# Kernel tuning notes

Hardware: AMD Instinct MI355X
Metric: run time of the kernel (lower is better)

Reference implementation:

```python
import jax, jax.numpy as jnp
import numpy as np

N = 100000    # nodes
R = 8         # relations
HFR = 128     # input feature dim
HTO = 128     # output feature dim
NNZ = 1600000 # edges (nonzeros of the (N*R, N) sparse matrix)


def setup_inputs() -> dict:
    key = jax.random.key(0)
    k1, k2, k3, k4, k5 = jax.random.split(key, 5)
    nodes = jax.random.normal(k1, (N, HFR), dtype=jnp.float32)
    rows = jax.random.randint(k2, (NNZ,), 0, N * R)   # row index into (N*R, N) sparse matrix
    cols = jax.random.randint(k3, (NNZ,), 0, N)       # column = source node
    indices = jnp.stack([rows, cols]).astype(jnp.int64)
    values = jax.random.uniform(k4, (NNZ,), dtype=jnp.float32)
    # xavier-uniform-ish init for (r, hfr, hto) relation weights
    weights = jax.random.normal(k5, (R, HFR, HTO), dtype=jnp.float32) * np.float32(1.0 / np.sqrt(HFR))
    return {"nodes": nodes, "indices": indices, "values": values, "weights": weights}


def reference(nodes, indices, values, weights):
    # nodes: [n, hfr]; indices: [2, nnz]; values: [nnz]; weights: [r, hfr, hto]
    n = nodes.shape[0]
    r = weights.shape[0]
    rows, cols = indices[0], indices[1]
    # spmm: (n*r, n) sparse @ (n, hfr) dense -> (n*r, hfr)
    msgs = values[:, None] * nodes[cols]                      # [nnz, hfr] gather + scale
    agg = jax.ops.segment_sum(msgs, rows, num_segments=n * r)  # [n*r, hfr] scatter-add
    agg = agg.reshape(r, n, -1)                                # [r, n, hfr]
    # per-relation GEMM 'rij,rnj->nri' followed by sum over r, fused into one einsum
    out = jnp.einsum('rij,rnj->ni', weights, agg)              # [n, hto]
    return jax.nn.relu(out)
```

## Files before the change

kernel.cpp:

```cpp
#include <hip/hip_runtime.h>
#include <hip/hip_bf16.h>
#include <stdint.h>

#define HFR 128
#define HTO 128
#define LDN 136

typedef short short8 __attribute__((ext_vector_type(8)));
typedef float f32x4  __attribute__((ext_vector_type(4)));
typedef unsigned long long u64;

static __device__ __forceinline__ unsigned short f2bf(float x) {
    __hip_bfloat16 h = __float2bfloat16(x);
    return *reinterpret_cast<unsigned short*>(&h);
}
static __device__ __forceinline__ float bflo(unsigned int x) {
    return __uint_as_float(x << 16);
}
static __device__ __forceinline__ float bfhi(unsigned int x) {
    return __uint_as_float(x & 0xffff0000u);
}

__global__ __launch_bounds__(256) void zero_i32(int* __restrict__ p, int n) {
    int i = blockIdx.x * 256 + threadIdx.x;
    if (i < n) p[i] = 0;
}

__global__ __launch_bounds__(256)
void count_kernel(const int* __restrict__ rows, int* __restrict__ cnt,
                  int N, int nnz) {
    int e = blockIdx.x * 256 + threadIdx.x;
    if (e >= nnz) return;
    int row = rows[e];
    int r   = row / N;
    int dst = row - r * N;
    atomicAdd(&cnt[dst], 1);
}

__global__ __launch_bounds__(256)
void scan_reduce(const int* __restrict__ cnt, int* __restrict__ bsum, int N) {
    __shared__ int s[256];
    int t = threadIdx.x;
    int i = blockIdx.x * 256 + t;
    s[t] = (i < N) ? cnt[i] : 0;
    __syncthreads();
    for (int off = 128; off > 0; off >>= 1) {
        if (t < off) s[t] += s[t + off];
        __syncthreads();
    }
    if (t == 0) bsum[blockIdx.x] = s[0];
}

__global__ __launch_bounds__(1024)
void scan_block(int* __restrict__ bsum, int nb) {
    __shared__ int s[1024];
    int t = threadIdx.x;
    s[t] = (t < nb) ? bsum[t] : 0;
    __syncthreads();
    for (int off = 1; off < 1024; off <<= 1) {
        int o = (t >= off) ? s[t - off] : 0;
        __syncthreads();
        s[t] += o;
        __syncthreads();
    }
    if (t < nb) bsum[t] = (t == 0) ? 0 : s[t - 1];
}

__global__ __launch_bounds__(256)
void scan_final(int* __restrict__ cnt, const int* __restrict__ bsum, int N) {
    __shared__ int s[256];
    int t = threadIdx.x;
    int i = blockIdx.x * 256 + t;
    int v = (i < N) ? cnt[i] : 0;
    s[t] = v;
    __syncthreads();
    for (int off = 1; off < 256; off <<= 1) {
        int o = (t >= off) ? s[t - off] : 0;
        __syncthreads();
        s[t] += o;
        __syncthreads();
    }
    int ex = ((t == 0) ? 0 : s[t - 1]) + bsum[blockIdx.x];
    if (i < N) cnt[i] = ex;
}

__global__ __launch_bounds__(256, 2)
void fused_tp(const float* __restrict__ nodes,
              const float* __restrict__ weights,
              __hip_bfloat16* __restrict__ H,
              const int* __restrict__ rows, const int* __restrict__ cols,
              const float* __restrict__ vals,
              int* __restrict__ cursor, u64* __restrict__ sorted,
              int N, int R, int nnz, int Tblocks) {
    __shared__ unsigned short nd[128 * LDN];
    __shared__ unsigned short wt[128 * LDN];

    if ((int)blockIdx.x >= Tblocks) {
        int e = (blockIdx.x - Tblocks) * 256 + threadIdx.x;
        if (e >= nnz) return;
        int row = rows[e];
        int r   = row / N;
        int dst = row - r * N;
        int pos = atomicAdd(&cursor[dst], 1);
        unsigned int lo = (unsigned int)cols[e] | ((unsigned int)r << 17);
        u64 rec = ((u64)__float_as_uint(vals[e]) << 32) | (u64)lo;
        sorted[pos] = rec;
        return;
    }

    const int t    = threadIdx.x;
    const int n0   = blockIdx.x * 128;
    const int lane = t & 63;
    const int w    = t >> 6;
    const int m    = lane & 15;
    const int quad = lane >> 4;
    const int q8   = quad * 8;
    const int w32  = w * 32;

    const float4* src4 = reinterpret_cast<const float4*>(nodes);
#pragma unroll
    for (int it = 0; it < 8; ++it) {
        int id  = t + 256 * it;
        int row = id >> 4;
        int k8  = id & 15;
        float4 v0 = make_float4(0.f, 0.f, 0.f, 0.f);
        float4 v1 = v0;
        if (n0 + row < N) {
            v0 = src4[(size_t)(n0 + row) * 32 + k8 * 2];
            v1 = src4[(size_t)(n0 + row) * 32 + k8 * 2 + 1];
        }
        short8 sv;
        sv[0] = f2bf(v0.x); sv[1] = f2bf(v0.y); sv[2] = f2bf(v0.z); sv[3] = f2bf(v0.w);
        sv[4] = f2bf(v1.x); sv[5] = f2bf(v1.y); sv[6] = f2bf(v1.z); sv[7] = f2bf(v1.w);
        *reinterpret_cast<short8*>(&nd[row * LDN + k8 * 8]) = sv;
    }

    for (int r = 0; r < R; ++r) {
        __syncthreads();
        const float4* wsrc = reinterpret_cast<const float4*>(weights + (size_t)r * HFR * HTO);
#pragma unroll
        for (int it = 0; it < 8; ++it) {
            int id  = t + 256 * it;
            int row = id >> 4;
            int k8  = id & 15;
            float4 v0 = wsrc[row * 32 + k8 * 2];
            float4 v1 = wsrc[row * 32 + k8 * 2 + 1];
            short8 sv;
            sv[0] = f2bf(v0.x); sv[1] = f2bf(v0.y); sv[2] = f2bf(v0.z); sv[3] = f2bf(v0.w);
            sv[4] = f2bf(v1.x); sv[5] = f2bf(v1.y); sv[6] = f2bf(v1.z); sv[7] = f2bf(v1.w);
            *reinterpret_cast<short8*>(&wt[row * LDN + k8 * 8]) = sv;
        }
        __syncthreads();

        f32x4 acc[2][8];
#pragma unroll
        for (int t2 = 0; t2 < 2; ++t2)
#pragma unroll
            for (int j = 0; j < 8; ++j) acc[t2][j] = (f32x4)(0.f);

#pragma unroll
        for (int kk = 0; kk < HFR; kk += 32) {
            short8 a0 = *reinterpret_cast<const short8*>(&nd[(w32 +      m) * LDN + kk + q8]);
            short8 a1 = *reinterpret_cast<const short8*>(&nd[(w32 + 16 + m) * LDN + kk + q8]);
#pragma unroll
            for (int j = 0; j < 8; ++j) {
                short8 b = *reinterpret_cast<const short8*>(&wt[(j * 16 + m) * LDN + kk + q8]);
                acc[0][j] = __builtin_amdgcn_mfma_f32_16x16x32_bf16(a0, b, acc[0][j], 0, 0, 0);
                acc[1][j] = __builtin_amdgcn_mfma_f32_16x16x32_bf16(a1, b, acc[1][j], 0, 0, 0);
            }
        }

#pragma unroll
        for (int t2 = 0; t2 < 2; ++t2) {
            int rowbase = n0 + w32 + t2 * 16 + quad * 4;
#pragma unroll
            for (int reg = 0; reg < 4; ++reg) {
                int n = rowbase + reg;
                if (n < N) {
                    __hip_bfloat16* dst = H + ((size_t)r * N + n) * HTO + m;
#pragma unroll
                    for (int j = 0; j < 8; ++j)
                        dst[j * 16] = __float2bfloat16(acc[t2][j][reg]);
                }
            }
        }
    }
}

__global__ __launch_bounds__(256)
void gather_kernel(const u64* __restrict__ sorted,
                   const int* __restrict__ cursor,
                   const __hip_bfloat16* __restrict__ H,
                   float* __restrict__ out, int N) {
    const int wave = threadIdx.x >> 6;
    const int lane = threadIdx.x & 63;
    const int n = blockIdx.x * 4 + wave;
    if (n >= N) return;

    int e         = (n == 0) ? 0 : cursor[n - 1];
    const int end = cursor[n];

    float a0 = 0.f, a1 = 0.f, b0 = 0.f, b1 = 0.f;
    float c0 = 0.f, c1 = 0.f, d0 = 0.f, d1 = 0.f;

    const unsigned short* Hu = reinterpret_cast<const unsigned short*>(H);

#define HROW(q) reinterpret_cast<const unsigned int*>( \
        Hu + ((((size_t)((unsigned int)(q) >> 17) & 7) * (size_t)N + \
               ((unsigned int)(q) & 0x1FFFF)) << 7))
#define VAL(q)  __uint_as_float((unsigned int)((q) >> 32))

    for (; e + 8 <= end; e += 8) {
        const u64* p = sorted + __builtin_amdgcn_readfirstlane(e);
        u64 q0 = p[0], q1 = p[1], q2 = p[2], q3 = p[3];
        u64 q4 = p[4], q5 = p[5], q6 = p[6], q7 = p[7];
        unsigned int x0 = HROW(q0)[lane];
        unsigned int x1 = HROW(q1)[lane];
        unsigned int x2 = HROW(q2)[lane];
        unsigned int x3 = HROW(q3)[lane];
        unsigned int x4 = HROW(q4)[lane];
        unsigned int x5 = HROW(q5)[lane];
        unsigned int x6 = HROW(q6)[lane];
        unsigned int x7 = HROW(q7)[lane];
        a0 = fmaf(bflo(x0), VAL(q0), a0); a1 = fmaf(bfhi(x0), VAL(q0), a1);
        b0 = fmaf(bflo(x1), VAL(q1), b0); b1 = fmaf(bfhi(x1), VAL(q1), b1);
        c0 = fmaf(bflo(x2), VAL(q2), c0); c1 = fmaf(bfhi(x2), VAL(q2), c1);
        d0 = fmaf(bflo(x3), VAL(q3), d0); d1 = fmaf(bfhi(x3), VAL(q3), d1);
        a0 = fmaf(bflo(x4), VAL(q4), a0); a1 = fmaf(bfhi(x4), VAL(q4), a1);
        b0 = fmaf(bflo(x5), VAL(q5), b0); b1 = fmaf(bfhi(x5), VAL(q5), b1);
        c0 = fmaf(bflo(x6), VAL(q6), c0); c1 = fmaf(bfhi(x6), VAL(q6), c1);
        d0 = fmaf(bflo(x7), VAL(q7), d0); d1 = fmaf(bfhi(x7), VAL(q7), d1);
    }
    for (; e + 2 <= end; e += 2) {
        const u64* p = sorted + __builtin_amdgcn_readfirstlane(e);
        u64 q0 = p[0], q1 = p[1];
        unsigned int x0 = HROW(q0)[lane];
        unsigned int x1 = HROW(q1)[lane];
        a0 = fmaf(bflo(x0), VAL(q0), a0); a1 = fmaf(bfhi(x0), VAL(q0), a1);
        b0 = fmaf(bflo(x1), VAL(q1), b0); b1 = fmaf(bfhi(x1), VAL(q1), b1);
    }
    if (e < end) {
        u64 q0 = sorted[e];
        unsigned int x0 = HROW(q0)[lane];
        a0 = fmaf(bflo(x0), VAL(q0), a0); a1 = fmaf(bfhi(x0), VAL(q0), a1);
    }
#undef HROW
#undef VAL

    float2 o;
    o.x = fmaxf(a0 + b0 + c0 + d0, 0.f);
    o.y = fmaxf(a1 + b1 + c1 + d1, 0.f);
    *reinterpret_cast<float2*>(out + (size_t)n * HTO + lane * 2) = o;
}

extern "C" void kernel_launch(void* const* d_in, const int* in_sizes, int n_in,
                              void* d_out, int out_size, void* d_ws, size_t ws_size,
                              hipStream_t stream) {
    const float* nodes   = (const float*)d_in[0];
    const int*   indices = (const int*)d_in[1];
    const float* vals    = (const float*)d_in[2];
    const float* weights = (const float*)d_in[3];

    const int N   = in_sizes[0] / HFR;
    const int nnz = in_sizes[1] / 2;
    const int R   = in_sizes[3] / (HFR * HTO);

    const int* rows = indices;
    const int* cols = indices + nnz;

    char* ws = (char*)d_ws;
    __hip_bfloat16* H = (__hip_bfloat16*)ws;
    size_t off = (size_t)R * N * HTO * sizeof(__hip_bfloat16);
    u64* sorted = (u64*)(ws + off);
    off += (size_t)nnz * sizeof(u64);
    int* cnt = (int*)(ws + off);
    off += (size_t)N * sizeof(int);
    int* bsum = (int*)(ws + off);

    float* out = (float*)d_out;

    const int NB = (N + 255) / 256;
    const int Tblocks = (N + 127) / 128;
    const int Pblocks = (nnz + 255) / 256;

    zero_i32<<<NB, 256, 0, stream>>>(cnt, N);
    count_kernel<<<Pblocks, 256, 0, stream>>>(rows, cnt, N, nnz);
    scan_reduce<<<NB, 256, 0, stream>>>(cnt, bsum, N);
    scan_block<<<1, 1024, 0, stream>>>(bsum, NB);
    scan_final<<<NB, 256, 0, stream>>>(cnt, bsum, N);
    fused_tp<<<Tblocks + Pblocks, 256, 0, stream>>>(nodes, weights, H,
                                                    rows, cols, vals,
                                                    cnt, sorted, N, R, nnz, Tblocks);
    gather_kernel<<<(N + 3) / 4, 256, 0, stream>>>(sorted, cnt, H, out, N);
}
```

Before: 381.1 us.

## Reorder to aggregate-then-transform with per-relation segment sort and fused GEMM reduction

Switches from computing per-relation transformed features then gathering, to first gathering bf16 node features into per-(relation,node) aggregates and then running one GEMM that sums over relations with ReLU in the epilogue. Sorting is now by full row index over N*R segments, and nodes/weights are pre-converted to bf16 in a prep kernel. Random gathers now hit a much smaller bf16 node table, but an extra full read of the aggregate buffer and many short segments are introduced. The output buffer is reused as scratch for counts and converted nodes.

```diff
diff --git a/kernel.cpp b/kernel.cpp
--- a/kernel.cpp
+++ b/kernel.cpp
@@ -21,28 +21,48 @@
     return __uint_as_float(x & 0xffff0000u);
 }
 
-__global__ __launch_bounds__(256) void zero_i32(int* __restrict__ p, int n) {
-    int i = blockIdx.x * 256 + threadIdx.x;
-    if (i < n) p[i] = 0;
-}
-
-__global__ __launch_bounds__(256)
-void count_kernel(const int* __restrict__ rows, int* __restrict__ cnt,
-                  int N, int nnz) {
+__global__ __launch_bounds__(256)
+void prep_kernel(const float* __restrict__ nodes, const float* __restrict__ weights,
+                 int* __restrict__ cnt, unsigned short* __restrict__ nb,
+                 unsigned short* __restrict__ wb,
+                 int nseg, int nfeat, int nw, int ZB, int CB) {
+    int b = blockIdx.x;
+    if (b < ZB) {
+        int i = (b * 256 + threadIdx.x) * 4;
+        if (i < nseg) {
+            int4 z = make_int4(0, 0, 0, 0);
+            *reinterpret_cast<int4*>(cnt + i) = z;
+        }
+        return;
+    }
+    const float* src; unsigned short* dst; int i, lim;
+    if (b < ZB + CB) { src = nodes;   dst = nb; i = ((b - ZB) * 256 + threadIdx.x) * 8;      lim = nfeat; }
+    else             { src = weights; dst = wb; i = ((b - ZB - CB) * 256 + threadIdx.x) * 8; lim = nw; }
+    if (i < lim) {
+        const float4* s = reinterpret_cast<const float4*>(src + i);
+        float4 v0 = s[0], v1 = s[1];
+        short8 sv;
+        sv[0] = f2bf(v0.x); sv[1] = f2bf(v0.y); sv[2] = f2bf(v0.z); sv[3] = f2bf(v0.w);
+        sv[4] = f2bf(v1.x); sv[5] = f2bf(v1.y); sv[6] = f2bf(v1.z); sv[7] = f2bf(v1.w);
+        *reinterpret_cast<short8*>(dst + i) = sv;
+    }
+}
+
+__global__ __launch_bounds__(256)
+void count_kernel(const int* __restrict__ rows, int* __restrict__ cnt, int nnz) {
     int e = blockIdx.x * 256 + threadIdx.x;
-    if (e >= nnz) return;
-    int row = rows[e];
-    int r   = row / N;
-    int dst = row - r * N;
-    atomicAdd(&cnt[dst], 1);
-}
-
-__global__ __launch_bounds__(256)
-void scan_reduce(const int* __restrict__ cnt, int* __restrict__ bsum, int N) {
+    if (e < nnz) atomicAdd(&cnt[rows[e]], 1);
+}
+
+__global__ __launch_bounds__(256)
+void scan_reduce(const int* __restrict__ cnt, int* __restrict__ bsum, int n) {
     __shared__ int s[256];
     int t = threadIdx.x;
-    int i = blockIdx.x * 256 + t;
-    s[t] = (i < N) ? cnt[i] : 0;
+    int i = blockIdx.x * 1024 + t * 4;
+    int v = 0;
+    if (i + 3 < n) { int4 q = *reinterpret_cast<const int4*>(cnt + i); v = q.x + q.y + q.z + q.w; }
+    else { for (int k = 0; k < 4; ++k) if (i + k < n) v += cnt[i + k]; }
+    s[t] = v;
     __syncthreads();
     for (int off = 128; off > 0; off >>= 1) {
         if (t < off) s[t] += s[t + off];
@@ -67,12 +87,20 @@
 }
 
 __global__ __launch_bounds__(256)
-void scan_final(int* __restrict__ cnt, const int* __restrict__ bsum, int N) {
+void scan_final(int* __restrict__ cnt, const int* __restrict__ bsum, int n) {
     __shared__ int s[256];
     int t = threadIdx.x;
-    int i = blockIdx.x * 256 + t;
-    int v = (i < N) ? cnt[i] : 0;
-    s[t] = v;
+    int i = blockIdx.x * 1024 + t * 4;
+    int4 q = make_int4(0, 0, 0, 0);
+    if (i + 3 < n) q = *reinterpret_cast<const int4*>(cnt + i);
+    else {
+        if (i     < n) q.x = cnt[i];
+        if (i + 1 < n) q.y = cnt[i + 1];
+        if (i + 2 < n) q.z = cnt[i + 2];
+        if (i + 3 < n) q.w = cnt[i + 3];
+    }
+    int tot = q.x + q.y + q.z + q.w;
+    s[t] = tot;
     __syncthreads();
     for (int off = 1; off < 256; off <<= 1) {
         int o = (t >= off) ? s[t - off] : 0;
@@ -81,32 +109,76 @@
         __syncthreads();
     }
     int ex = ((t == 0) ? 0 : s[t - 1]) + bsum[blockIdx.x];
-    if (i < N) cnt[i] = ex;
+    int4 w;
+    w.x = ex; w.y = ex + q.x; w.z = w.y + q.y; w.w = w.z + q.z;
+    if (i + 3 < n) *reinterpret_cast<int4*>(cnt + i) = w;
+    else {
+        if (i     < n) cnt[i]     = w.x;
+        if (i + 1 < n) cnt[i + 1] = w.y;
+        if (i + 2 < n) cnt[i + 2] = w.z;
+        if (i + 3 < n) cnt[i + 3] = w.w;
+    }
+}
+
+__global__ __launch_bounds__(256)
+void place_kernel(const int* __restrict__ rows, const int* __restrict__ cols,
+                  const float* __restrict__ vals,
+                  int* __restrict__ cnt, u64* __restrict__ sorted, int nnz) {
+    int e = blockIdx.x * 256 + threadIdx.x;
+    if (e >= nnz) return;
+    int pos = atomicAdd(&cnt[rows[e]], 1);
+    sorted[pos] = ((u64)__float_as_uint(vals[e]) << 32) | (u64)(unsigned int)cols[e];
+}
+
+__global__ __launch_bounds__(256)
+void gather_kernel(const u64* __restrict__ sorted, const int* __restrict__ cnt,
+                   const unsigned short* __restrict__ nb,
+                   unsigned int* __restrict__ agg, int nseg) {
+    const int wave = threadIdx.x >> 6;
+    const int lane = threadIdx.x & 63;
+    const int s = blockIdx.x * 4 + wave;
+    if (s >= nseg) return;
+
+    int e         = (s == 0) ? 0 : cnt[s - 1];
+    const int end = cnt[s];
+
+    float a0 = 0.f, a1 = 0.f, b0 = 0.f, b1 = 0.f;
+    float c0 = 0.f, c1 = 0.f, d0 = 0.f, d1 = 0.f;
+
+#define NROW(q) (reinterpret_cast<const unsigned int*>(nb + (((size_t)(unsigned int)(q)) << 7)))
+#define VAL(q)  __uint_as_float((unsigned int)((q) >> 32))
+    for (; e + 4 <= end; e += 4) {
+        const u64* p = sorted + __builtin_amdgcn_readfirstlane(e);
+        u64 q0 = p[0], q1 = p[1], q2 = p[2], q3 = p[3];
+        unsigned int x0 = NROW(q0)[lane];
+        unsigned int x1 = NROW(q1)[lane];
+        unsigned int x2 = NROW(q2)[lane];
+        unsigned int x3 = NROW(q3)[lane];
+        a0 = fmaf(bflo(x0), VAL(q0), a0); a1 = fmaf(bfhi(x0), VAL(q0), a1);
+        b0 = fmaf(bflo(x1), VAL(q1), b0); b1 = fmaf(bfhi(x1), VAL(q1), b1);
+        c0 = fmaf(bflo(x2), VAL(q2), c0); c1 = fmaf(bfhi(x2), VAL(q2), c1);
+        d0 = fmaf(bflo(x3), VAL(q3), d0); d1 = fmaf(bfhi(x3), VAL(q3), d1);
+    }
+    for (; e < end; ++e) {
+        u64 q0 = sorted[e];
+        unsigned int x0 = NROW(q0)[lane];
+        a0 = fmaf(bflo(x0), VAL(q0), a0); a1 = fmaf(bfhi(x0), VAL(q0), a1);
+    }
+#undef NROW
+#undef VAL
+
+    float r0 = a0 + b0 + c0 + d0;
+    float r1 = a1 + b1 + c1 + d1;
+    unsigned int pk = ((unsigned int)f2bf(r1) << 16) | (unsigned int)f2bf(r0);
+    agg[((size_t)s << 6) + lane] = pk;
 }
 
 __global__ __launch_bounds__(256, 2)
-void fused_tp(const float* __restrict__ nodes,
-              const float* __restrict__ weights,
-              __hip_bfloat16* __restrict__ H,
-              const int* __restrict__ rows, const int* __restrict__ cols,
-              const float* __restrict__ vals,
-              int* __restrict__ cursor, u64* __restrict__ sorted,
-              int N, int R, int nnz, int Tblocks) {
+void gemm_kernel(const unsigned short* __restrict__ agg,
+                 const unsigned short* __restrict__ wb,
+                 float* __restrict__ out, int N, int R) {
     __shared__ unsigned short nd[128 * LDN];
     __shared__ unsigned short wt[128 * LDN];
-
-    if ((int)blockIdx.x >= Tblocks) {
-        int e = (blockIdx.x - Tblocks) * 256 + threadIdx.x;
-        if (e >= nnz) return;
-        int row = rows[e];
-        int r   = row / N;
-        int dst = row - r * N;
-        int pos = atomicAdd(&cursor[dst], 1);
-        unsigned int lo = (unsigned int)cols[e] | ((unsigned int)r << 17);
-        u64 rec = ((u64)__float_as_uint(vals[e]) << 32) | (u64)lo;
-        sorted[pos] = rec;
-        return;
-    }
 
     const int t    = threadIdx.x;
     const int n0   = blockIdx.x * 128;
@@ -117,46 +189,29 @@
     const int q8   = quad * 8;
     const int w32  = w * 32;
 
-    const float4* src4 = reinterpret_cast<const float4*>(nodes);
-#pragma unroll
-    for (int it = 0; it < 8; ++it) {
-        int id  = t + 256 * it;
-        int row = id >> 4;
-        int k8  = id & 15;
-        float4 v0 = make_float4(0.f, 0.f, 0.f, 0.f);
-        float4 v1 = v0;
-        if (n0 + row < N) {
-            v0 = src4[(size_t)(n0 + row) * 32 + k8 * 2];
-            v1 = src4[(size_t)(n0 + row) * 32 + k8 * 2 + 1];
-        }
-        short8 sv;
-        sv[0] = f2bf(v0.x); sv[1] = f2bf(v0.y); sv[2] = f2bf(v0.z); sv[3] = f2bf(v0.w);
-        sv[4] = f2bf(v1.x); sv[5] = f2bf(v1.y); sv[6] = f2bf(v1.z); sv[7] = f2bf(v1.w);
-        *reinterpret_cast<short8*>(&nd[row * LDN + k8 * 8]) = sv;
-    }
+    f32x4 acc[2][8];
+#pragma unroll
+    for (int t2 = 0; t2 < 2; ++t2)
+#pragma unroll
+        for (int j = 0; j < 8; ++j) acc[t2][j] = (f32x4)(0.f);
 
     for (int r = 0; r < R; ++r) {
         __syncthreads();
-        const float4* wsrc = reinterpret_cast<const float4*>(weights + (size_t)r * HFR * HTO);
+        const unsigned short* asrc = agg + ((size_t)r * N + n0) * HFR;
+        const unsigned short* wsrc = wb + (size_t)r * HFR * HTO;
 #pragma unroll
         for (int it = 0; it < 8; ++it) {
             int id  = t + 256 * it;
             int row = id >> 4;
             int k8  = id & 15;
-            float4 v0 = wsrc[row * 32 + k8 * 2];
-            float4 v1 = wsrc[row * 32 + k8 * 2 + 1];
-            short8 sv;
-            sv[0] = f2bf(v0.x); sv[1] = f2bf(v0.y); sv[2] = f2bf(v0.z); sv[3] = f2bf(v0.w);
-            sv[4] = f2bf(v1.x); sv[5] = f2bf(v1.y); sv[6] = f2bf(v1.z); sv[7] = f2bf(v1.w);
-            *reinterpret_cast<short8*>(&wt[row * LDN + k8 * 8]) = sv;
-        }
-        __syncthreads();
-
-        f32x4 acc[2][8];
-#pragma unroll
-        for (int t2 = 0; t2 < 2; ++t2)
-#pragma unroll
-            for (int j = 0; j < 8; ++j) acc[t2][j] = (f32x4)(0.f);
+            short8 sv = (short8)0;
+            if (n0 + row < N)
+                sv = *reinterpret_cast<const short8*>(asrc + row * HFR + k8 * 8);
+            *reinterpret_cast<short8*>(&nd[row * LDN + k8 * 8]) = sv;
+            short8 wv = *reinterpret_cast<const short8*>(wsrc + row * HFR + k8 * 8);
+            *reinterpret_cast<short8*>(&wt[row * LDN + k8 * 8]) = wv;
+        }
+        __syncthreads();
 
 #pragma unroll
         for (int kk = 0; kk < HFR; kk += 32) {
@@ -169,88 +224,38 @@
                 acc[1][j] = __builtin_amdgcn_mfma_f32_16x16x32_bf16(a1, b, acc[1][j], 0, 0, 0);
             }
         }
-
-#pragma unroll
-        for (int t2 = 0; t2 < 2; ++t2) {
-            int rowbase = n0 + w32 + t2 * 16 + quad * 4;
-#pragma unroll
-            for (int reg = 0; reg < 4; ++reg) {
-                int n = rowbase + reg;
-                if (n < N) {
-                    __hip_bfloat16* dst = H + ((size_t)r * N + n) * HTO + m;
+    }
+
+    float* lf = reinterpret_cast<float*>(wt);
+    for (int h = 0; h < 2; ++h) {
+        __syncthreads();
+        if ((w >> 1) == h) {
+            int lbase = (w & 1) * 32;
+#pragma unroll
+            for (int t2 = 0; t2 < 2; ++t2)
+#pragma unroll
+                for (int reg = 0; reg < 4; ++reg) {
+                    int lr = lbase + t2 * 16 + quad * 4 + reg;
 #pragma unroll
                     for (int j = 0; j < 8; ++j)
-                        dst[j * 16] = __float2bfloat16(acc[t2][j][reg]);
+                        lf[lr * 132 + m + 16 * j] = acc[t2][j][reg];
                 }
+        }
+        __syncthreads();
+#pragma unroll
+        for (int it = 0; it < 8; ++it) {
+            int id  = t + 256 * it;
+            int row = id >> 5;
+            int k4  = id & 31;
+            int n = n0 + h * 64 + row;
+            if (n < N) {
+                float4 v = *reinterpret_cast<const float4*>(&lf[row * 132 + k4 * 4]);
+                v.x = fmaxf(v.x, 0.f); v.y = fmaxf(v.y, 0.f);
+                v.z = fmaxf(v.z, 0.f); v.w = fmaxf(v.w, 0.f);
+                *reinterpret_cast<float4*>(out + (size_t)n * HTO + k4 * 4) = v;
             }
         }
     }
-}
-
-__global__ __launch_bounds__(256)
-void gather_kernel(const u64* __restrict__ sorted,
-                   const int* __restrict__ cursor,
-                   const __hip_bfloat16* __restrict__ H,
-                   float* __restrict__ out, int N) {
-    const int wave = threadIdx.x >> 6;
-    const int lane = threadIdx.x & 63;
-    const int n = blockIdx.x * 4 + wave;
-    if (n >= N) return;
-
-    int e         = (n == 0) ? 0 : cursor[n - 1];
-    const int end = cursor[n];
-
-    float a0 = 0.f, a1 = 0.f, b0 = 0.f, b1 = 0.f;
-    float c0 = 0.f, c1 = 0.f, d0 = 0.f, d1 = 0.f;
-
-    const unsigned short* Hu = reinterpret_cast<const unsigned short*>(H);
-
-#define HROW(q) reinterpret_cast<const unsigned int*>( \
-        Hu + ((((size_t)((unsigned int)(q) >> 17) & 7) * (size_t)N + \
-               ((unsigned int)(q) & 0x1FFFF)) << 7))
-#define VAL(q)  __uint_as_float((unsigned int)((q) >> 32))
-
-    for (; e + 8 <= end; e += 8) {
-        const u64* p = sorted + __builtin_amdgcn_readfirstlane(e);
-        u64 q0 = p[0], q1 = p[1], q2 = p[2], q3 = p[3];
-        u64 q4 = p[4], q5 = p[5], q6 = p[6], q7 = p[7];
-        unsigned int x0 = HROW(q0)[lane];
-        unsigned int x1 = HROW(q1)[lane];
-        unsigned int x2 = HROW(q2)[lane];
-        unsigned int x3 = HROW(q3)[lane];
-        unsigned int x4 = HROW(q4)[lane];
-        unsigned int x5 = HROW(q5)[lane];
-        unsigned int x6 = HROW(q6)[lane];
-        unsigned int x7 = HROW(q7)[lane];
-        a0 = fmaf(bflo(x0), VAL(q0), a0); a1 = fmaf(bfhi(x0), VAL(q0), a1);
-        b0 = fmaf(bflo(x1), VAL(q1), b0); b1 = fmaf(bfhi(x1), VAL(q1), b1);
-        c0 = fmaf(bflo(x2), VAL(q2), c0); c1 = fmaf(bfhi(x2), VAL(q2), c1);
-        d0 = fmaf(bflo(x3), VAL(q3), d0); d1 = fmaf(bfhi(x3), VAL(q3), d1);
-        a0 = fmaf(bflo(x4), VAL(q4), a0); a1 = fmaf(bfhi(x4), VAL(q4), a1);
-        b0 = fmaf(bflo(x5), VAL(q5), b0); b1 = fmaf(bfhi(x5), VAL(q5), b1);
-        c0 = fmaf(bflo(x6), VAL(q6), c0); c1 = fmaf(bfhi(x6), VAL(q6), c1);
-        d0 = fmaf(bflo(x7), VAL(q7), d0); d1 = fmaf(bfhi(x7), VAL(q7), d1);
-    }
-    for (; e + 2 <= end; e += 2) {
-        const u64* p = sorted + __builtin_amdgcn_readfirstlane(e);
-        u64 q0 = p[0], q1 = p[1];
-        unsigned int x0 = HROW(q0)[lane];
-        unsigned int x1 = HROW(q1)[lane];
-        a0 = fmaf(bflo(x0), VAL(q0), a0); a1 = fmaf(bfhi(x0), VAL(q0), a1);
-        b0 = fmaf(bflo(x1), VAL(q1), b0); b1 = fmaf(bfhi(x1), VAL(q1), b1);
-    }
-    if (e < end) {
-        u64 q0 = sorted[e];
-        unsigned int x0 = HROW(q0)[lane];
-        a0 = fmaf(bflo(x0), VAL(q0), a0); a1 = fmaf(bfhi(x0), VAL(q0), a1);
-    }
-#undef HROW
-#undef VAL
-
-    float2 o;
-    o.x = fmaxf(a0 + b0 + c0 + d0, 0.f);
-    o.y = fmaxf(a1 + b1 + c1 + d1, 0.f);
-    *reinterpret_cast<float2*>(out + (size_t)n * HTO + lane * 2) = o;
 }
 
 extern "C" void kernel_launch(void* const* d_in, const int* in_sizes, int n_in,
@@ -261,35 +266,43 @@
     const float* vals    = (const float*)d_in[2];
     const float* weights = (const float*)d_in[3];
 
-    const int N   = in_sizes[0] / HFR;
-    const int nnz = in_sizes[1] / 2;
-    const int R   = in_sizes[3] / (HFR * HTO);
+    const int N    = in_sizes[0] / HFR;
+    const int nnz  = in_sizes[1] / 2;
+    const int R    = in_sizes[3] / (HFR * HTO);
+    const int nseg = N * R;
 
     const int* rows = indices;
     const int* cols = indices + nnz;
 
     char* ws = (char*)d_ws;
-    __hip_bfloat16* H = (__hip_bfloat16*)ws;
-    size_t off = (size_t)R * N * HTO * sizeof(__hip_bfloat16);
+    unsigned short* agg = (unsigned short*)ws;
+    size_t off = (size_t)nseg * HFR * sizeof(unsigned short);
     u64* sorted = (u64*)(ws + off);
     off += (size_t)nnz * sizeof(u64);
-    int* cnt = (int*)(ws + off);
-    off += (size_t)N * sizeof(int);
     int* bsum = (int*)(ws + off);
+    off += 4096;
+    unsigned short* wb = (unsigned short*)(ws + off);
 
     float* out = (float*)d_out;
-
-    const int NB = (N + 255) / 256;
-    const int Tblocks = (N + 127) / 128;
-    const int Pblocks = (nnz + 255) / 256;
-
-    zero_i32<<<NB, 256, 0, stream>>>(cnt, N);
-    count_kernel<<<Pblocks, 256, 0, stream>>>(rows, cnt, N, nnz);
-    scan_reduce<<<NB, 256, 0, stream>>>(cnt, bsum, N);
+    int* cnt = (int*)d_out;
+    unsigned short* nb = (unsigned short*)((char*)d_out + (4 << 20));
+
+    const int nfeat = N * HFR;
+    const int nw    = R * HFR * HTO;
+    const int ZB = (nseg + 1023) / 1024;
+    const int CB = (nfeat + 2047) / 2048;
+    const int WB = (nw + 2047) / 2048;
+    const int EB = (nnz + 255) / 256;
+    const int NB = (nseg + 1023) / 1024;
+
+    prep_kernel<<<ZB + CB + WB, 256, 0, stream>>>(nodes, weights, cnt, nb, wb,
+                                                  nseg, nfeat, nw, ZB, CB);
+    count_kernel<<<EB, 256, 0, stream>>>(rows, cnt, nnz);
+    scan_reduce<<<NB, 256, 0, stream>>>(cnt, bsum, nseg);
     scan_block<<<1, 1024, 0, stream>>>(bsum, NB);
-    scan_final<<<NB, 256, 0, stream>>>(cnt, bsum, N);
-    fused_tp<<<Tblocks + Pblocks, 256, 0, stream>>>(nodes, weights, H,
-                                                    rows, cols, vals,
-                                                    cnt, sorted, N, R, nnz, Tblocks);
-    gather_kernel<<<(N + 3) / 4, 256, 0, stream>>>(sorted, cnt, H, out, N);
-}
+    scan_final<<<NB, 256, 0, stream>>>(cnt, bsum, nseg);
+    place_kernel<<<EB, 256, 0, stream>>>(rows, cols, vals, cnt, sorted, nnz);
+    gather_kernel<<<(nseg + 3) / 4, 256, 0, stream>>>(sorted, cnt,
+                                                      nb, (unsigned int*)agg, nseg);
+    gemm_kernel<<<(N + 127) / 128, 256, 0, stream>>>(agg, wb, out, N, R);
+}
```

Result: slower. 539.1 us (+41.5%).

## Stage GEMM output through LDS for coalesced H stores and split gather per half-row

Applied to the files above, without the earlier changes.

The transform kernel now writes its bf16 accumulators into shared memory first, then copies H out with 16-byte coalesced row stores. Previously it issued scattered 2-byte global stores. The gather kernel assigns two waves per destination node, each covering 64 features with 16-bit loads, which doubles wave parallelism. In exchange, every wave reads the sorted edge records again. The zero and scan kernels are also vectorised to handle four counts per thread with int4 accesses, which cuts their block counts.

```diff
diff --git a/kernel.cpp b/kernel.cpp
--- a/kernel.cpp
+++ b/kernel.cpp
@@ -14,16 +14,13 @@
     __hip_bfloat16 h = __float2bfloat16(x);
     return *reinterpret_cast<unsigned short*>(&h);
 }
-static __device__ __forceinline__ float bflo(unsigned int x) {
-    return __uint_as_float(x << 16);
-}
-static __device__ __forceinline__ float bfhi(unsigned int x) {
-    return __uint_as_float(x & 0xffff0000u);
+static __device__ __forceinline__ float bf2f(unsigned short x) {
+    return __uint_as_float((unsigned int)x << 16);
 }
 
 __global__ __launch_bounds__(256) void zero_i32(int* __restrict__ p, int n) {
-    int i = blockIdx.x * 256 + threadIdx.x;
-    if (i < n) p[i] = 0;
+    int i = (blockIdx.x * 256 + threadIdx.x) * 4;
+    if (i < n) *reinterpret_cast<int4*>(p + i) = make_int4(0, 0, 0, 0);
 }
 
 __global__ __launch_bounds__(256)
@@ -33,16 +30,18 @@
     if (e >= nnz) return;
     int row = rows[e];
     int r   = row / N;
-    int dst = row - r * N;
-    atomicAdd(&cnt[dst], 1);
+    atomicAdd(&cnt[row - r * N], 1);
 }
 
 __global__ __launch_bounds__(256)
-void scan_reduce(const int* __restrict__ cnt, int* __restrict__ bsum, int N) {
+void scan_reduce(const int* __restrict__ cnt, int* __restrict__ bsum, int n) {
     __shared__ int s[256];
     int t = threadIdx.x;
-    int i = blockIdx.x * 256 + t;
-    s[t] = (i < N) ? cnt[i] : 0;
+    int i = blockIdx.x * 1024 + t * 4;
+    int v = 0;
+    if (i + 3 < n) { int4 q = *reinterpret_cast<const int4*>(cnt + i); v = q.x + q.y + q.z + q.w; }
+    else { for (int k = 0; k < 4; ++k) if (i + k < n) v += cnt[i + k]; }
+    s[t] = v;
     __syncthreads();
     for (int off = 128; off > 0; off >>= 1) {
         if (t < off) s[t] += s[t + off];
@@ -67,12 +66,19 @@
 }
 
 __global__ __launch_bounds__(256)
-void scan_final(int* __restrict__ cnt, const int* __restrict__ bsum, int N) {
+void scan_final(int* __restrict__ cnt, const int* __restrict__ bsum, int n) {
     __shared__ int s[256];
     int t = threadIdx.x;
-    int i = blockIdx.x * 256 + t;
-    int v = (i < N) ? cnt[i] : 0;
-    s[t] = v;
+    int i = blockIdx.x * 1024 + t * 4;
+    int4 q = make_int4(0, 0, 0, 0);
+    if (i + 3 < n) q = *reinterpret_cast<const int4*>(cnt + i);
+    else {
+        if (i     < n) q.x = cnt[i];
+        if (i + 1 < n) q.y = cnt[i + 1];
+        if (i + 2 < n) q.z = cnt[i + 2];
+    }
+    int tot = q.x + q.y + q.z + q.w;
+    s[t] = tot;
     __syncthreads();
     for (int off = 1; off < 256; off <<= 1) {
         int o = (t >= off) ? s[t - off] : 0;
@@ -81,7 +87,14 @@
         __syncthreads();
     }
     int ex = ((t == 0) ? 0 : s[t - 1]) + bsum[blockIdx.x];
-    if (i < N) cnt[i] = ex;
+    int4 w;
+    w.x = ex; w.y = ex + q.x; w.z = w.y + q.y; w.w = w.z + q.z;
+    if (i + 3 < n) *reinterpret_cast<int4*>(cnt + i) = w;
+    else {
+        if (i     < n) cnt[i]     = w.x;
+        if (i + 1 < n) cnt[i + 1] = w.y;
+        if (i + 2 < n) cnt[i + 2] = w.z;
+    }
 }
 
 __global__ __launch_bounds__(256, 2)
@@ -103,8 +116,7 @@
         int dst = row - r * N;
         int pos = atomicAdd(&cursor[dst], 1);
         unsigned int lo = (unsigned int)cols[e] | ((unsigned int)r << 17);
-        u64 rec = ((u64)__float_as_uint(vals[e]) << 32) | (u64)lo;
-        sorted[pos] = rec;
+        sorted[pos] = ((u64)__float_as_uint(vals[e]) << 32) | (u64)lo;
         return;
     }
 
@@ -170,87 +182,91 @@
             }
         }
 
+        __syncthreads();
 #pragma unroll
         for (int t2 = 0; t2 < 2; ++t2) {
-            int rowbase = n0 + w32 + t2 * 16 + quad * 4;
-#pragma unroll
-            for (int reg = 0; reg < 4; ++reg) {
-                int n = rowbase + reg;
-                if (n < N) {
-                    __hip_bfloat16* dst = H + ((size_t)r * N + n) * HTO + m;
-#pragma unroll
-                    for (int j = 0; j < 8; ++j)
-                        dst[j * 16] = __float2bfloat16(acc[t2][j][reg]);
-                }
-            }
+            int rowb = w32 + t2 * 16 + quad * 4;
+#pragma unroll
+            for (int reg = 0; reg < 4; ++reg)
+#pragma unroll
+                for (int j = 0; j < 8; ++j)
+                    wt[(rowb + reg) * LDN + 16 * j + m] = f2bf(acc[t2][j][reg]);
+        }
+        __syncthreads();
+        __hip_bfloat16* hdst = H + (size_t)r * N * HTO;
+#pragma unroll
+        for (int it = 0; it < 8; ++it) {
+            int id  = t + 256 * it;
+            int row = id >> 4;
+            int k8  = id & 15;
+            if (n0 + row < N)
+                *reinterpret_cast<short8*>(
+                    reinterpret_cast<unsigned short*>(hdst) +
+                    ((size_t)(n0 + row) << 7) + k8 * 8) =
+                    *reinterpret_cast<const short8*>(&wt[row * LDN + k8 * 8]);
         }
     }
 }
 
 __global__ __launch_bounds__(256)
 void gather_kernel(const u64* __restrict__ sorted,
-                   const int* __restrict__ cursor,
-                   const __hip_bfloat16* __restrict__ H,
+                   const int* __restrict__ cnt,
+                   const unsigned short* __restrict__ Hu,
                    float* __restrict__ out, int N) {
-    const int wave = threadIdx.x >> 6;
+    const int gw   = blockIdx.x * 4 + (threadIdx.x >> 6);
     const int lane = threadIdx.x & 63;
-    const int n = blockIdx.x * 4 + wave;
+    const int n    = gw >> 1;
+    const int half = gw & 1;
     if (n >= N) return;
 
-    int e         = (n == 0) ? 0 : cursor[n - 1];
-    const int end = cursor[n];
-
-    float a0 = 0.f, a1 = 0.f, b0 = 0.f, b1 = 0.f;
-    float c0 = 0.f, c1 = 0.f, d0 = 0.f, d1 = 0.f;
-
-    const unsigned short* Hu = reinterpret_cast<const unsigned short*>(H);
-
-#define HROW(q) reinterpret_cast<const unsigned int*>( \
-        Hu + ((((size_t)((unsigned int)(q) >> 17) & 7) * (size_t)N + \
-               ((unsigned int)(q) & 0x1FFFF)) << 7))
-#define VAL(q)  __uint_as_float((unsigned int)((q) >> 32))
+    int e         = (n == 0) ? 0 : cnt[n - 1];
+    const int end = cnt[n];
+    const int fo  = half * 64 + lane;
+
+    float a0 = 0.f, b0 = 0.f, c0 = 0.f, d0 = 0.f;
+
+#define HIDX(q) (((((size_t)(((unsigned int)(q) >> 17) & 7)) * (size_t)N + \
+                   (size_t)((unsigned int)(q) & 0x1FFFF)) << 7) + fo)
+#define VALF(q) __uint_as_float((unsigned int)((q) >> 32))
 
     for (; e + 8 <= end; e += 8) {
         const u64* p = sorted + __builtin_amdgcn_readfirstlane(e);
         u64 q0 = p[0], q1 = p[1], q2 = p[2], q3 = p[3];
         u64 q4 = p[4], q5 = p[5], q6 = p[6], q7 = p[7];
-        unsigned int x0 = HROW(q0)[lane];
-        unsigned int x1 = HROW(q1)[lane];
-        unsigned int x2 = HROW(q2)[lane];
-        unsigned int x3 = HROW(q3)[lane];
-        unsigned int x4 = HROW(q4)[lane];
-        unsigned int x5 = HROW(q5)[lane];
-        unsigned int x6 = HROW(q6)[lane];
-        unsigned int x7 = HROW(q7)[lane];
-        a0 = fmaf(bflo(x0), VAL(q0), a0); a1 = fmaf(bfhi(x0), VAL(q0), a1);
-        b0 = fmaf(bflo(x1), VAL(q1), b0); b1 = fmaf(bfhi(x1), VAL(q1), b1);
-        c0 = fmaf(bflo(x2), VAL(q2), c0); c1 = fmaf(bfhi(x2), VAL(q2), c1);
-        d0 = fmaf(bflo(x3), VAL(q3), d0); d1 = fmaf(bfhi(x3), VAL(q3), d1);
-        a0 = fmaf(bflo(x4), VAL(q4), a0); a1 = fmaf(bfhi(x4), VAL(q4), a1);
-        b0 = fmaf(bflo(x5), VAL(q5), b0); b1 = fmaf(bfhi(x5), VAL(q5), b1);
-        c0 = fmaf(bflo(x6), VAL(q6), c0); c1 = fmaf(bfhi(x6), VAL(q6), c1);
-        d0 = fmaf(bflo(x7), VAL(q7), d0); d1 = fmaf(bfhi(x7), VAL(q7), d1);
+        unsigned short x0 = Hu[HIDX(q0)];
+        unsigned short x1 = Hu[HIDX(q1)];
+        unsigned short x2 = Hu[HIDX(q2)];
+        unsigned short x3 = Hu[HIDX(q3)];
+        unsigned short x4 = Hu[HIDX(q4)];
+        unsigned short x5 = Hu[HIDX(q5)];
+        unsigned short x6 = Hu[HIDX(q6)];
+        unsigned short x7 = Hu[HIDX(q7)];
+        a0 = fmaf(bf2f(x0), VALF(q0), a0);
+        b0 = fmaf(bf2f(x1), VALF(q1), b0);
+        c0 = fmaf(bf2f(x2), VALF(q2), c0);
+        d0 = fmaf(bf2f(x3), VALF(q3), d0);
+        a0 = fmaf(bf2f(x4), VALF(q4), a0);
+        b0 = fmaf(bf2f(x5), VALF(q5), b0);
+        c0 = fmaf(bf2f(x6), VALF(q6), c0);
+        d0 = fmaf(bf2f(x7), VALF(q7), d0);
     }
     for (; e + 2 <= end; e += 2) {
         const u64* p = sorted + __builtin_amdgcn_readfirstlane(e);
         u64 q0 = p[0], q1 = p[1];
-        unsigned int x0 = HROW(q0)[lane];
-        unsigned int x1 = HROW(q1)[lane];
-        a0 = fmaf(bflo(x0), VAL(q0), a0); a1 = fmaf(bfhi(x0), VAL(q0), a1);
-        b0 = fmaf(bflo(x1), VAL(q1), b0); b1 = fmaf(bfhi(x1), VAL(q1), b1);
+        unsigned short x0 = Hu[HIDX(q0)];
+        unsigned short x1 = Hu[HIDX(q1)];
+        a0 = fmaf(bf2f(x0), VALF(q0), a0);
+        b0 = fmaf(bf2f(x1), VALF(q1), b0);
     }
     if (e < end) {
         u64 q0 = sorted[e];
-        unsigned int x0 = HROW(q0)[lane];
-        a0 = fmaf(bflo(x0), VAL(q0), a0); a1 = fmaf(bfhi(x0), VAL(q0), a1);
-    }
-#undef HROW
-#undef VAL
-
-    float2 o;
-    o.x = fmaxf(a0 + b0 + c0 + d0, 0.f);
-    o.y = fmaxf(a1 + b1 + c1 + d1, 0.f);
-    *reinterpret_cast<float2*>(out + (size_t)n * HTO + lane * 2) = o;
+        unsigned short x0 = Hu[HIDX(q0)];
+        a0 = fmaf(bf2f(x0), VALF(q0), a0);
+    }
+#undef HIDX
+#undef VALF
+
+    out[(size_t)n * HTO + fo] = fmaxf(a0 + b0 + c0 + d0, 0.f);
 }
 
 extern "C" void kernel_launch(void* const* d_in, const int* in_sizes, int n_in,
@@ -279,17 +295,18 @@
 
     float* out = (float*)d_out;
 
-    const int NB = (N + 255) / 256;
+    const int NB      = (N + 1023) / 1024;
+    const int EB      = (nnz + 255) / 256;
     const int Tblocks = (N + 127) / 128;
-    const int Pblocks = (nnz + 255) / 256;
 
     zero_i32<<<NB, 256, 0, stream>>>(cnt, N);
-    count_kernel<<<Pblocks, 256, 0, stream>>>(rows, cnt, N, nnz);
+    count_kernel<<<EB, 256, 0, stream>>>(rows, cnt, N, nnz);
     scan_reduce<<<NB, 256, 0, stream>>>(cnt, bsum, N);
     scan_block<<<1, 1024, 0, stream>>>(bsum, NB);
     scan_final<<<NB, 256, 0, stream>>>(cnt, bsum, N);
-    fused_tp<<<Tblocks + Pblocks, 256, 0, stream>>>(nodes, weights, H,
-                                                    rows, cols, vals,
-                                                    cnt, sorted, N, R, nnz, Tblocks);
-    gather_kernel<<<(N + 3) / 4, 256, 0, stream>>>(sorted, cnt, H, out, N);
-}
+    fused_tp<<<Tblocks + EB, 256, 0, stream>>>(nodes, weights, H,
+                                               rows, cols, vals,
+                                               cnt, sorted, N, R, nnz, Tblocks);
+    gather_kernel<<<(2 * N + 3) / 4, 256, 0, stream>>>(
+        sorted, cnt, (const unsigned short*)H, out, N);
+}
```

New measurement: 419.2 us. 10.0% more time.
